# Performance work log

Hardware: AMD Instinct MI355X
Metric: run time of the kernel (lower is better)

Reference implementation:

```python
import jax, jax.numpy as jnp
import numpy as np

N = 8192        # batch_size == num nodes == num hyperedges
D = 512         # hidden_dim
H_HEADS = 8
HD = D // H_HEADS
TOP_K = 16
EPS = 1e-5      # LayerNorm eps


def setup_inputs() -> dict:
    key = jax.random.key(0)
    ks = jax.random.split(key, 10)
    def rn(k, shape, scale=0.02):
        return jax.random.normal(k, shape, dtype=jnp.float32) * scale
    return {
        "x0": jax.random.normal(ks[0], (N, D), dtype=jnp.float32),
        "x1": jax.random.normal(ks[1], (N, D), dtype=jnp.float32),
        # modality projections: Linear -> ReLU -> LayerNorm (per modality)
        "w_p0": rn(ks[2], (D, D)), "b_p0": jnp.zeros((D,), jnp.float32),
        "g0": jnp.ones((D,), jnp.float32), "beta0": jnp.zeros((D,), jnp.float32),
        "w_p1": rn(ks[3], (D, D)), "b_p1": jnp.zeros((D,), jnp.float32),
        "g1": jnp.ones((D,), jnp.float32), "beta1": jnp.zeros((D,), jnp.float32),
        # MultiheadAttention packed in-proj + out-proj
        "in_w": rn(ks[4], (3 * D, D)), "in_b": jnp.zeros((3 * D,), jnp.float32),
        "out_w": rn(ks[5], (D, D)), "out_b": jnp.zeros((D,), jnp.float32),
        # edge weight predictor MLP
        "ew_w1": rn(ks[6], (D // 2, D)), "ew_b1": jnp.zeros((D // 2,), jnp.float32),
        "ew_w2": rn(ks[7], (1, D // 2)), "ew_b2": jnp.zeros((1,), jnp.float32),
    }


def _layernorm(x, g, b):
    m = x.mean(-1, keepdims=True)
    v = ((x - m) ** 2).mean(-1, keepdims=True)
    return (x - m) * jax.lax.rsqrt(v + EPS) * g + b


def _forward(x0, x1, w_p0, b_p0, g0, beta0, w_p1, b_p1, g1, beta1,
             in_w, in_b, out_w, out_b, ew_w1, ew_b1, ew_w2, ew_b2):
    # per-modality projection: Linear -> ReLU -> LayerNorm
    p0 = _layernorm(jax.nn.relu(x0 @ w_p0.T + b_p0), g0, beta0)
    p1 = _layernorm(jax.nn.relu(x1 @ w_p1.T + b_p1), g1, beta1)
    seq = jnp.stack([p0, p1], axis=1)                       # [N, 2, D]
    # cross-modal MHA (self-attention over the 2 modality tokens)
    qkv = seq @ in_w.T + in_b                               # [N, 2, 3D]
    q, k, v = jnp.split(qkv, 3, axis=-1)
    q = q.reshape(N, 2, H_HEADS, HD)
    k = k.reshape(N, 2, H_HEADS, HD)
    v = v.reshape(N, 2, H_HEADS, HD)
    scores = jnp.einsum('bqhd,bkhd->bhqk', q, k) / jnp.sqrt(jnp.float32(HD))
    attn = jax.nn.softmax(scores, axis=-1)                  # [N, h, 2, 2]
    ctx = jnp.einsum('bhqk,bkhd->bqhd', attn, v).reshape(N, 2, D)
    attended = ctx @ out_w.T + out_b                        # [N, 2, D]
    fused = attended.mean(axis=1)                           # [N, D]
    # node-node attention similarity, row-softmax
    sim = jax.nn.softmax(fused @ fused.T, axis=1)           # [N, N]
    _, idx = jax.lax.top_k(sim, TOP_K)                      # [N, K]
    vals = jnp.take_along_axis(sim, idx, axis=1)            # [N, K]
    rows = jnp.arange(N)
    # H[i,i]=1 first, then H[neighbor, i] = sim[i, neighbor] (may overwrite diag)
    H = jnp.zeros((N, N), sim.dtype).at[rows, rows].set(1.0)
    H = H.at[idx, rows[:, None]].set(vals)
    colsum = H.sum(axis=0)
    H = H.at[rows, rows].set(jnp.where(colsum == 0, 1.0, H[rows, rows]))
    # edge weights
    hidden = jax.nn.relu(fused @ ew_w1.T + ew_b1)
    ew = jax.nn.sigmoid(hidden @ ew_w2.T + ew_b2)[:, 0]     # [N]
    ew = jnp.maximum(ew, 1e-8)
    return H, ew


def reference(x0, x1, w_p0, b_p0, g0, beta0, w_p1, b_p1, g1, beta1,
              in_w, in_b, out_w, out_b, ew_w1, ew_b1, ew_w2, ew_b2):
    return _forward(x0, x1, w_p0, b_p0, g0, beta0, w_p1, b_p1, g1, beta1,
                    in_w, in_b, out_w, out_b, ew_w1, ew_b1, ew_w2, ew_b2)
```

## Files before the change

### kernel.cpp

```cpp
#include <hip/hip_runtime.h>
#include <hip/hip_bf16.h>

#define NN 8192
#define DD 512

typedef unsigned short u16;
typedef __bf16 bf16_t;
typedef bf16_t bf16x8 __attribute__((ext_vector_type(8)));
typedef float f32x4 __attribute__((ext_vector_type(4)));

__device__ __forceinline__ float bf2f(u16 h) {
    union { unsigned u; float f; } v; v.u = ((unsigned)h) << 16; return v.f;
}
__device__ __forceinline__ float bflo(unsigned u) {
    union { unsigned u; float f; } v; v.u = u << 16; return v.f;
}
__device__ __forceinline__ float bfhi(unsigned u) {
    union { unsigned u; float f; } v; v.u = u & 0xFFFF0000u; return v.f;
}
__device__ __forceinline__ u16 f2bf(float f) {
    union { float f; unsigned u; } v; v.f = f;
    unsigned r = v.u + 0x7fffu + ((v.u >> 16) & 1u);
    return (u16)(r >> 16);
}

#define PIPE_BARRIER(N) do { \
    __builtin_amdgcn_sched_barrier(0); \
    asm volatile("s_waitcnt vmcnt(" #N ")" ::: "memory"); \
    __builtin_amdgcn_s_barrier(); \
    __builtin_amdgcn_sched_barrier(0); \
} while (0)

__global__ __launch_bounds__(256) void cvt5(
        const float* __restrict__ s0, u16* __restrict__ d0,
        const float* __restrict__ s1, u16* __restrict__ d1,
        const float* __restrict__ s2, u16* __restrict__ d2,
        const float* __restrict__ s3, u16* __restrict__ d3,
        const float* __restrict__ s4, u16* __restrict__ d4) {
    size_t v = ((size_t)blockIdx.x * 256 + threadIdx.x) * 8;
    const float* s; u16* d; size_t off;
    if (v < 262144)       { s = s0; d = d0; off = v; }
    else if (v < 524288)  { s = s1; d = d1; off = v - 262144; }
    else if (v < 1310720) { s = s2; d = d2; off = v - 524288; }
    else if (v < 1572864) { s = s3; d = d3; off = v - 1310720; }
    else                  { s = s4; d = d4; off = v - 1572864; }
    float4 a = *(const float4*)(s + off);
    float4 b = *(const float4*)(s + off + 4);
    ushort4 o0 = make_ushort4(f2bf(a.x), f2bf(a.y), f2bf(a.z), f2bf(a.w));
    ushort4 o1 = make_ushort4(f2bf(b.x), f2bf(b.y), f2bf(b.z), f2bf(b.w));
    *(ushort4*)(d + off) = o0;
    *(ushort4*)(d + off + 4) = o1;
}

#define EPS_LDS 136
__global__ __launch_bounds__(256) void gemm_proj(
        const float* __restrict__ X0, const float* __restrict__ X1,
        const u16* __restrict__ B0, const float* __restrict__ bias0,
        const u16* __restrict__ B1, const float* __restrict__ bias1,
        u16* __restrict__ C) {
    __shared__ alignas(16) u16 Smem[2][16384];
    const int t = threadIdx.x;
    const int lane = t & 63;
    const int wave = t >> 6;
    const int wm = (wave >> 1) * 64;
    const int wn = (wave & 1) * 64;
    const int rowA = blockIdx.y * 128;
    const int rowB = blockIdx.x * 128;
    const bool mod1 = (int)blockIdx.y >= 64;
    const float* A32 = mod1 ? X1 + (size_t)(rowA - 8192) * DD
                            : X0 + (size_t)rowA * DD;
    const u16* B = mod1 ? B1 : B0;
    const float* bias = mod1 ? bias1 : bias0;

    f32x4 acc[4][4] = {};
    const int mrow = lane & 15;
    const int kk = (lane >> 4) * 8;
    const int trow = t >> 3;
    const int koff = (t & 7) * 8;

    float ar[4][8];
    auto LOADA = [&](int k0) {
        #pragma unroll
        for (int r = 0; r < 4; ++r) {
            const float* s = A32 + (size_t)(r * 32 + trow) * DD + k0 + koff;
            float4 f0 = *(const float4*)s;
            float4 f1 = *(const float4*)(s + 4);
            ar[r][0] = f0.x; ar[r][1] = f0.y; ar[r][2] = f0.z; ar[r][3] = f0.w;
            ar[r][4] = f1.x; ar[r][5] = f1.y; ar[r][6] = f1.z; ar[r][7] = f1.w;
        }
    };
    auto WRITEA = [&](int buf) {
        u16* As = Smem[buf];
        #pragma unroll
        for (int r = 0; r < 4; ++r) {
            int chunk = r * 256 + t;
            ushort4 o0 = make_ushort4(f2bf(ar[r][0]), f2bf(ar[r][1]),
                                      f2bf(ar[r][2]), f2bf(ar[r][3]));
            ushort4 o1 = make_ushort4(f2bf(ar[r][4]), f2bf(ar[r][5]),
                                      f2bf(ar[r][6]), f2bf(ar[r][7]));
            *(ushort4*)(As + chunk * 8) = o0;
            *(ushort4*)(As + chunk * 8 + 4) = o1;
        }
    };
    auto BSTAGE = [&](int buf, int k0) {
        u16* Bs = Smem[buf] + 8192;
        #pragma unroll
        for (int r = 0; r < 4; ++r) {
            int chunk = r * 256 + t;
            const u16* srcB = B + (size_t)(rowB + (chunk >> 3)) * DD + k0 + (chunk & 7) * 8;
            __builtin_amdgcn_global_load_lds(
                (const __attribute__((address_space(1))) void*)srcB,
                (__attribute__((address_space(3))) void*)(Bs + chunk * 8), 16, 0, 0);
        }
    };

    LOADA(0); BSTAGE(0, 0); WRITEA(0);
    __syncthreads();
    int cur = 0;
    for (int ti = 0; ti < 8; ++ti) {
        if (ti < 7) { LOADA((ti + 1) << 6); BSTAGE(cur ^ 1, (ti + 1) << 6); }
        const u16* As = Smem[cur];
        const u16* Bs = Smem[cur] + 8192;
        #pragma unroll
        for (int ks = 0; ks < 64; ks += 32) {
            bf16x8 af[4], bfv[4];
            #pragma unroll
            for (int i = 0; i < 4; ++i)
                af[i] = *(const bf16x8*)(As + (wm + i * 16 + mrow) * 64 + ks + kk);
            #pragma unroll
            for (int j = 0; j < 4; ++j)
                bfv[j] = *(const bf16x8*)(Bs + (wn + j * 16 + mrow) * 64 + ks + kk);
            #pragma unroll
            for (int i = 0; i < 4; ++i)
                #pragma unroll
                for (int j = 0; j < 4; ++j)
                    acc[i][j] = __builtin_amdgcn_mfma_f32_16x16x32_bf16(af[i], bfv[j], acc[i][j], 0, 0, 0);
        }
        if (ti < 7) WRITEA(cur ^ 1);
        __syncthreads();
        cur ^= 1;
    }

    u16* Ep = &Smem[0][0];
    const int er0 = wm + (lane >> 4) * 4;
    const int ec0 = wn + (lane & 15);
    #pragma unroll
    for (int j = 0; j < 4; ++j) {
        int c = ec0 + j * 16;
        float bv = bias[rowB + c];
        #pragma unroll
        for (int i = 0; i < 4; ++i) {
            #pragma unroll
            for (int r = 0; r < 4; ++r) {
                float v = fmaxf(acc[i][j][r] + bv, 0.0f);
                Ep[(er0 + i * 16 + r) * EPS_LDS + c] = f2bf(v);
            }
        }
    }
    __syncthreads();
    #pragma unroll
    for (int pass = 0; pass < 8; ++pass) {
        int chunk = pass * 256 + t;
        int rloc = chunk >> 4, coff = (chunk & 15) * 8;
        bf16x8 v = *(const bf16x8*)(Ep + rloc * EPS_LDS + coff);
        *(bf16x8*)(C + (size_t)(rowA + rloc) * DD + rowB + coff) = v;
    }
}

__global__ __launch_bounds__(256) void gemm_qkv(const u16* __restrict__ A,
        const u16* __restrict__ B, const float* __restrict__ bias,
        u16* __restrict__ V, float* __restrict__ AL) {
    __shared__ alignas(16) u16 Smem[3][8192];
    const int t = threadIdx.x;
    const int lane = t & 63;
    const int wave = t >> 6;
    const int wm = (wave >> 1) * 64;
    const int wn = (wave & 1) * 64;
    const int c = blockIdx.x;
    const int rowA = blockIdx.y * 128;
    const bool isQK = (c < 8);

    f32x4 acc[4][4] = {};
    const int mrow = lane & 15;
    const int kk = (lane >> 4) * 8;

    auto STAGE = [&](int buf, int k0) {
        u16* As = Smem[buf];
        u16* Bs = Smem[buf] + 4096;
        #pragma unroll
        for (int r = 0; r < 2; ++r) {
            int chunk = r * 256 + t;
            int rr = chunk >> 2;
            int ko = (chunk & 3) * 8;
            int brow = isQK ? (c * 64 + rr + ((rr >= 64) ? 448 : 0))
                            : (1024 + (c - 8) * 128 + rr);
            const u16* srcA = A + (size_t)(rowA + rr) * DD + k0 + ko;
            __builtin_amdgcn_global_load_lds(
                (const __attribute__((address_space(1))) void*)srcA,
                (__attribute__((address_space(3))) void*)(As + chunk * 8), 16, 0, 0);
            const u16* srcB = B + (size_t)brow * DD + k0 + ko;
            __builtin_amdgcn_global_load_lds(
                (const __attribute__((address_space(1))) void*)srcB,
                (__attribute__((address_space(3))) void*)(Bs + chunk * 8), 16, 0, 0);
        }
    };
    auto COMPUTE = [&](int buf) {
        const u16* As = Smem[buf];
        const u16* Bs = Smem[buf] + 4096;
        bf16x8 af[4], bfv[4];
        #pragma unroll
        for (int i = 0; i < 4; ++i)
            af[i] = *(const bf16x8*)(As + (wm + i * 16 + mrow) * 32 + kk);
        #pragma unroll
        for (int j = 0; j < 4; ++j)
            bfv[j] = *(const bf16x8*)(Bs + (wn + j * 16 + mrow) * 32 + kk);
        #pragma unroll
        for (int i = 0; i < 4; ++i)
            #pragma unroll
            for (int j = 0; j < 4; ++j)
                acc[i][j] = __builtin_amdgcn_mfma_f32_16x16x32_bf16(af[i], bfv[j], acc[i][j], 0, 0, 0);
    };

    STAGE(0, 0);
    STAGE(1, 32);
    PIPE_BARRIER(4);
    #pragma unroll
    for (int ts = 0; ts < 14; ++ts) {
        STAGE((ts + 2) % 3, (ts + 2) * 32);
        COMPUTE(ts % 3);
        PIPE_BARRIER(4);
    }
    COMPUTE(2);
    PIPE_BARRIER(0);
    COMPUTE(0);
    __syncthreads();

    u16* Ep = &Smem[0][0];
    const int er0 = wm + (lane >> 4) * 4;
    const int ec0 = wn + (lane & 15);
    #pragma unroll
    for (int j = 0; j < 4; ++j) {
        int cc = ec0 + j * 16;
        int bcol = isQK ? ((cc < 64) ? c * 64 + cc : 448 + c * 64 + cc)
                        : (1024 + (c - 8) * 128 + cc);
        float bv = bias[bcol];
        #pragma unroll
        for (int i = 0; i < 4; ++i) {
            #pragma unroll
            for (int r = 0; r < 4; ++r)
                Ep[(er0 + i * 16 + r) * EPS_LDS + cc] = f2bf(acc[i][j][r] + bv);
        }
    }
    __syncthreads();
    if (isQK) {
        int nd = t >> 2, cb = t & 3, tt2 = cb >> 1, ss = cb & 1;
        const u16* qrow = Ep + (2 * nd + tt2) * EPS_LDS;
        const u16* krow = Ep + (2 * nd + ss) * EPS_LDS + 64;
        float s = 0.0f;
        #pragma unroll
        for (int d8 = 0; d8 < 8; ++d8) {
            bf16x8 qv = *(const bf16x8*)(qrow + d8 * 8);
            bf16x8 kv = *(const bf16x8*)(krow + d8 * 8);
            #pragma unroll
            for (int u = 0; u < 8; ++u) s += (float)qv[u] * (float)kv[u];
        }
        s *= 0.125f;
        float o = __shfl_xor(s, 1);
        float mm = fmaxf(s, o);
        float es = __expf(s - mm), eo = __expf(o - mm);
        float a = es / (es + eo);
        float a2 = __shfl_xor(a, 2);
        float al = 0.5f * (a + a2);
        if (cb < 2)
            AL[(size_t)(rowA / 2 + nd) * 16 + c * 2 + cb] = al;
    } else {
        #pragma unroll
        for (int pass = 0; pass < 8; ++pass) {
            int chunk = pass * 256 + t;
            int rloc = chunk >> 4, coff = (chunk & 15) * 8;
            bf16x8 v = *(const bf16x8*)(Ep + rloc * EPS_LDS + coff);
            *(bf16x8*)(V + (size_t)(rowA + rloc) * 512 + (c - 8) * 128 + coff) = v;
        }
    }
}

__global__ __launch_bounds__(256) void gemm_outp(
        const float* __restrict__ AL, const u16* __restrict__ V,
        const u16* __restrict__ W, const float* __restrict__ bias,
        u16* __restrict__ C) {
    __shared__ alignas(16) u16 Smem[2][16384];
    const int t = threadIdx.x;
    const int lane = t & 63;
    const int wave = t >> 6;
    const int wm = (wave >> 1) * 64;
    const int wn = (wave & 1) * 64;
    const int rowA = blockIdx.y * 128;
    const int rowB = blockIdx.x * 128;

    f32x4 acc[4][4] = {};
    const int mrow = lane & 15;
    const int kk = (lane >> 4) * 8;
    const int trow = t >> 3;
    const int koff = (t & 7) * 8;

    uint4 v0r[4], v1r[4];
    float2 alr[4];
    auto LOADA = [&](int ti) {
        #pragma unroll
        for (int r = 0; r < 4; ++r) {
            int node = rowA + r * 32 + trow;
            alr[r] = *(const float2*)(AL + (size_t)node * 16 + ti * 2);
            const u16* v0p = V + (size_t)(2 * node) * 512 + ti * 64 + koff;
            v0r[r] = *(const uint4*)v0p;
            v1r[r] = *(const uint4*)(v0p + 512);
        }
    };
    auto WRITEA = [&](int buf) {
        u16* As = Smem[buf];
        #pragma unroll
        for (int r = 0; r < 4; ++r) {
            int chunk = r * 256 + t;
            union { u16 us[8]; ushort4 u4[2]; } o;
            #pragma unroll
            for (int q = 0; q < 4; ++q) {
                unsigned w0 = (&v0r[r].x)[q], w1 = (&v1r[r].x)[q];
                o.us[q * 2]     = f2bf(alr[r].x * bflo(w0) + alr[r].y * bflo(w1));
                o.us[q * 2 + 1] = f2bf(alr[r].x * bfhi(w0) + alr[r].y * bfhi(w1));
            }
            *(ushort4*)(As + chunk * 8) = o.u4[0];
            *(ushort4*)(As + chunk * 8 + 4) = o.u4[1];
        }
    };
    auto BSTAGE = [&](int buf, int k0) {
        u16* Bs = Smem[buf] + 8192;
        #pragma unroll
        for (int r = 0; r < 4; ++r) {
            int chunk = r * 256 + t;
            const u16* srcB = W + (size_t)(rowB + (chunk >> 3)) * DD + k0 + (chunk & 7) * 8;
            __builtin_amdgcn_global_load_lds(
                (const __attribute__((address_space(1))) void*)srcB,
                (__attribute__((address_space(3))) void*)(Bs + chunk * 8), 16, 0, 0);
        }
    };

    LOADA(0); BSTAGE(0, 0); WRITEA(0);
    __syncthreads();
    int cur = 0;
    for (int ti = 0; ti < 8; ++ti) {
        if (ti < 7) { LOADA(ti + 1); BSTAGE(cur ^ 1, (ti + 1) << 6); }
        const u16* As = Smem[cur];
        const u16* Bs = Smem[cur] + 8192;
        #pragma unroll
        for (int ks = 0; ks < 64; ks += 32) {
            bf16x8 af[4], bfv[4];
            #pragma unroll
            for (int i = 0; i < 4; ++i)
                af[i] = *(const bf16x8*)(As + (wm + i * 16 + mrow) * 64 + ks + kk);
            #pragma unroll
            for (int j = 0; j < 4; ++j)
                bfv[j] = *(const bf16x8*)(Bs + (wn + j * 16 + mrow) * 64 + ks + kk);
            #pragma unroll
            for (int i = 0; i < 4; ++i)
                #pragma unroll
                for (int j = 0; j < 4; ++j)
                    acc[i][j] = __builtin_amdgcn_mfma_f32_16x16x32_bf16(af[i], bfv[j], acc[i][j], 0, 0, 0);
        }
        if (ti < 7) WRITEA(cur ^ 1);
        __syncthreads();
        cur ^= 1;
    }

    u16* Ep = &Smem[0][0];
    const int er0 = wm + (lane >> 4) * 4;
    const int ec0 = wn + (lane & 15);
    #pragma unroll
    for (int j = 0; j < 4; ++j) {
        int c = ec0 + j * 16;
        float bv = bias[rowB + c];
        #pragma unroll
        for (int i = 0; i < 4; ++i) {
            #pragma unroll
            for (int r = 0; r < 4; ++r)
                Ep[(er0 + i * 16 + r) * EPS_LDS + c] = f2bf(acc[i][j][r] + bv);
        }
    }
    __syncthreads();
    #pragma unroll
    for (int pass = 0; pass < 8; ++pass) {
        int chunk = pass * 256 + t;
        int rloc = chunk >> 4, coff = (chunk & 15) * 8;
        bf16x8 v = *(const bf16x8*)(Ep + rloc * EPS_LDS + coff);
        *(bf16x8*)(C + (size_t)(rowA + rloc) * DD + rowB + coff) = v;
    }
}

#define SYM_LDS 129
__global__ __launch_bounds__(256) void gemm_symh(const u16* __restrict__ F,
        u16* __restrict__ C, const u16* __restrict__ W1,
        const float* __restrict__ b1, u16* __restrict__ Hid) {
    __shared__ alignas(16) u16 Smem[3][8192];
    const int bx = blockIdx.x, by = blockIdx.y;
    const bool isHid = (bx >= 64);
    if (!isHid && bx < by) return;
    const int t = threadIdx.x;
    const int lane = t & 63;
    const int wave = t >> 6;
    const int wm = (wave >> 1) * 64;
    const int wn = (wave & 1) * 64;
    const int rowI = by * 128;
    const int rowJ = isHid ? (bx - 64) * 128 : bx * 128;
    const u16* Bsrc = isHid ? W1 : F;

    f32x4 acc[4][4] = {};
    const int mrow = lane & 15;
    const int kk = (lane >> 4) * 8;

    auto STAGE = [&](int buf, int k0) {
        u16* As = Smem[buf];
        u16* Bs = Smem[buf] + 4096;
        #pragma unroll
        for (int r = 0; r < 2; ++r) {
            int chunk = r * 256 + t;
            int row = chunk >> 2;
            int ko = (chunk & 3) * 8;
            const u16* srcA = F + (size_t)(rowI + row) * DD + k0 + ko;
            __builtin_amdgcn_global_load_lds(
                (const __attribute__((address_space(1))) void*)srcA,
                (__attribute__((address_space(3))) void*)(As + chunk * 8), 16, 0, 0);
            const u16* srcB = Bsrc + (size_t)(rowJ + row) * DD + k0 + ko;
            __builtin_amdgcn_global_load_lds(
                (const __attribute__((address_space(1))) void*)srcB,
                (__attribute__((address_space(3))) void*)(Bs + chunk * 8), 16, 0, 0);
        }
    };
    auto COMPUTE = [&](int buf) {
        const u16* As = Smem[buf];
        const u16* Bs = Smem[buf] + 4096;
        bf16x8 af[4], bfv[4];
        #pragma unroll
        for (int i = 0; i < 4; ++i)
            af[i] = *(const bf16x8*)(As + (wm + i * 16 + mrow) * 32 + kk);
        #pragma unroll
        for (int j = 0; j < 4; ++j)
            bfv[j] = *(const bf16x8*)(Bs + (wn + j * 16 + mrow) * 32 + kk);
        #pragma unroll
        for (int i = 0; i < 4; ++i)
            #pragma unroll
            for (int j = 0; j < 4; ++j)
                acc[i][j] = __builtin_amdgcn_mfma_f32_16x16x32_bf16(af[i], bfv[j], acc[i][j], 0, 0, 0);
    };

    STAGE(0, 0);
    STAGE(1, 32);
    PIPE_BARRIER(4);
    #pragma unroll
    for (int ts = 0; ts < 14; ++ts) {
        STAGE((ts + 2) % 3, (ts + 2) * 32);
        COMPUTE(ts % 3);
        PIPE_BARRIER(4);
    }
    COMPUTE(2);
    PIPE_BARRIER(0);
    COMPUTE(0);
    __syncthreads();

    u16* Ep = &Smem[0][0];
    const int er0 = wm + (lane >> 4) * 4;
    const int ec0 = wn + (lane & 15);
    #pragma unroll
    for (int j = 0; j < 4; ++j) {
        int c = ec0 + j * 16;
        float bv = isHid ? b1[rowJ + c] : 0.0f;
        #pragma unroll
        for (int i = 0; i < 4; ++i) {
            #pragma unroll
            for (int r = 0; r < 4; ++r) {
                float v = acc[i][j][r] + bv;
                if (isHid) v = fmaxf(v, 0.0f);
                Ep[(er0 + i * 16 + r) * SYM_LDS + c] = f2bf(v);
            }
        }
    }
    __syncthreads();
    if (isHid) {
        #pragma unroll
        for (int pass = 0; pass < 8; ++pass) {
            int chunk = pass * 256 + t;
            int rloc = chunk >> 4, coff = (chunk & 15) * 8;
            union { u16 us[8]; bf16x8 v; } buf;
            #pragma unroll
            for (int k = 0; k < 8; ++k) buf.us[k] = Ep[rloc * SYM_LDS + coff + k];
            *(bf16x8*)(Hid + (size_t)(rowI + rloc) * 256 + rowJ + coff) = buf.v;
        }
        return;
    }
    #pragma unroll
    for (int pass = 0; pass < 8; ++pass) {
        int chunk = pass * 256 + t;
        int rloc = chunk >> 4, coff = (chunk & 15) * 8;
        union { u16 us[8]; bf16x8 v; } buf;
        #pragma unroll
        for (int k = 0; k < 8; ++k) buf.us[k] = Ep[rloc * SYM_LDS + coff + k];
        *(bf16x8*)(C + (size_t)(rowI + rloc) * NN + rowJ + coff) = buf.v;
    }
    if (bx != by) {
        #pragma unroll
        for (int pass = 0; pass < 8; ++pass) {
            int chunk = pass * 256 + t;
            int tr = chunk >> 4, roff = (chunk & 15) * 8;
            union { u16 us[8]; bf16x8 v; } buf;
            #pragma unroll
            for (int k = 0; k < 8; ++k) buf.us[k] = Ep[(roff + k) * SYM_LDS + tr];
            *(bf16x8*)(C + (size_t)(rowJ + tr) * NN + rowI + roff) = buf.v;
        }
    }
}

__global__ __launch_bounds__(256) void ln2_kernel(const u16* __restrict__ y,
        const float* __restrict__ g0, const float* __restrict__ b0,
        const float* __restrict__ g1, const float* __restrict__ b1,
        u16* __restrict__ seq) {
    int n = blockIdx.x * 4 + (threadIdx.x >> 6);
    int lane = threadIdx.x & 63;
    int modality = n >> 13, node = n & (NN - 1);
    const float* g = modality ? g1 : g0;
    const float* b = modality ? b1 : b0;
    bf16x8 v = *(const bf16x8*)(y + (size_t)n * DD + lane * 8);
    float x[8];
    float s = 0.0f;
    #pragma unroll
    for (int u = 0; u < 8; ++u) { x[u] = (float)v[u]; s += x[u]; }
    #pragma unroll
    for (int off = 32; off; off >>= 1) s += __shfl_xor(s, off);
    float mean = s * (1.0f / DD);
    float vs = 0.0f;
    #pragma unroll
    for (int u = 0; u < 8; ++u) { x[u] -= mean; vs += x[u] * x[u]; }
    #pragma unroll
    for (int off = 32; off; off >>= 1) vs += __shfl_xor(vs, off);
    float inv = rsqrtf(vs * (1.0f / DD) + 1e-5f);
    float4 ga = *(const float4*)(g + lane * 8);
    float4 gb = *(const float4*)(g + lane * 8 + 4);
    float4 ba = *(const float4*)(b + lane * 8);
    float4 bb = *(const float4*)(b + lane * 8 + 4);
    union { u16 us[8]; bf16x8 v; } o;
    o.us[0] = f2bf(x[0] * inv * ga.x + ba.x);
    o.us[1] = f2bf(x[1] * inv * ga.y + ba.y);
    o.us[2] = f2bf(x[2] * inv * ga.z + ba.z);
    o.us[3] = f2bf(x[3] * inv * ga.w + ba.w);
    o.us[4] = f2bf(x[4] * inv * gb.x + bb.x);
    o.us[5] = f2bf(x[5] * inv * gb.y + bb.y);
    o.us[6] = f2bf(x[6] * inv * gb.z + bb.z);
    o.us[7] = f2bf(x[7] * inv * gb.w + bb.w);
    *(bf16x8*)(seq + (size_t)node * (2 * DD) + modality * DD + lane * 8) = o.v;
}

__global__ __launch_bounds__(256) void topk_bf16(u16* __restrict__ S,
        float* __restrict__ topv, int* __restrict__ topi,
        u16* __restrict__ hidden, const float* __restrict__ w2,
        const float* __restrict__ b2, float* __restrict__ ew_out,
        float* __restrict__ H) {
    const int blk = blockIdx.x;
    const int t = threadIdx.x;
    const float4 z4 = make_float4(0.f, 0.f, 0.f, 0.f);
    if (blk >= 2048) {
        int wv = t >> 6, lane = t & 63;
        int n0 = (blk - 2048) * 64 + wv * 16;
        float wa = w2[lane], wb = w2[lane + 64], wc = w2[lane + 128], wd = w2[lane + 192];
        for (int q = 0; q < 16; ++q) {
            int n = n0 + q;
            const u16* hr = hidden + (size_t)n * 256;
            float s = bf2f(hr[lane]) * wa + bf2f(hr[lane + 64]) * wb
                    + bf2f(hr[lane + 128]) * wc + bf2f(hr[lane + 192]) * wd;
            #pragma unroll
            for (int off = 32; off; off >>= 1) s += __shfl_xor(s, off);
            if (lane == 0) {
                float z = s + b2[0];
                float sig = 1.0f / (1.0f + __expf(-z));
                ew_out[n] = fmaxf(sig, 1e-8f);
            }
        }
        float4* zb = (float4*)(hidden + (size_t)n0 * 256);
        #pragma unroll
        for (int i = 0; i < 8; ++i) zb[i * 64 + lane] = z4;
        return;
    }
    const float NEG = -3e38f;
    const int SENT = 0x7FFFFFFF;
    int row = blk * 4 + (t >> 6);
    int lane = t & 63;
    u16* Sr = S + (size_t)row * NN;

    float m = NEG, l = 0.0f;
    float t1v = NEG, t2v = NEG, t3v = NEG;
    int t1i = SENT, t2i = SENT, t3i = SENT;

    #pragma unroll
    for (int p = 0; p < 16; ++p) {
        uint4 raw = *(const uint4*)(Sr + p * 512 + lane * 8);
        int base = p * 512 + lane * 8;
        #pragma unroll
        for (int q = 0; q < 4; ++q) {
            unsigned w = (&raw.x)[q];
            #pragma unroll
            for (int h = 0; h < 2; ++h) {
                float x = h ? bfhi(w) : bflo(w);
                int xi = base + q * 2 + h;
                if (x > m) { l = l * __expf(m - x) + 1.0f; m = x; }
                else l += __expf(x - m);
                bool g1 = x > t1v, g2 = x > t2v, g3 = x > t3v;
                t3v = g2 ? t2v : (g3 ? x : t3v);
                t3i = g2 ? t2i : (g3 ? xi : t3i);
                t2v = g1 ? t1v : (g2 ? x : t2v);
                t2i = g1 ? t1i : (g2 ? xi : t2i);
                t1v = g1 ? x : t1v;
                t1i = g1 ? xi : t1i;
            }
        }
    }
    #pragma unroll
    for (int off = 32; off; off >>= 1) {
        float om = __shfl_xor(m, off);
        float ol = __shfl_xor(l, off);
        float nm = fmaxf(m, om);
        l = l * __expf(m - nm) + ol * __expf(om - nm);
        m = nm;
    }

    unsigned mk0 = 0, mk1 = 0, mk2 = 0, mk3 = 0;
    float c1v = t1v, c2v = t2v, c3v = t3v;
    int c1i = t1i, c2i = t2i, c3i = t3i;
    for (int r = 0; r < 16; ++r) {
        float wv = c1v; int wi = c1i;
        #pragma unroll
        for (int off = 32; off; off >>= 1) {
            float ov = __shfl_xor(wv, off);
            int oi = __shfl_xor(wi, off);
            if (ov > wv || (ov == wv && oi < wi)) { wv = ov; wi = oi; }
        }
        if (lane == 0) {
            topv[(size_t)row * 16 + r] = __expf(wv - m) / l;
            topi[(size_t)row * 16 + r] = wi;
        }
        if (wi == c1i) {
            int slot = ((wi >> 9) << 3) | (wi & 7);
            unsigned bit = 1u << (slot & 31);
            if (slot < 32) mk0 |= bit; else if (slot < 64) mk1 |= bit;
            else if (slot < 96) mk2 |= bit; else mk3 |= bit;
            c1v = c2v; c1i = c2i;
            c2v = c3v; c2i = c3i;
            c3v = NEG; c3i = SENT;
            if (c1i == SENT) {
                float nb = NEG; int ni = SENT;
                #pragma unroll
                for (int p = 0; p < 16; ++p) {
                    uint4 raw = *(const uint4*)(Sr + p * 512 + lane * 8);
                    int base = p * 512 + lane * 8;
                    #pragma unroll
                    for (int q = 0; q < 4; ++q) {
                        unsigned w = (&raw.x)[q];
                        #pragma unroll
                        for (int h = 0; h < 2; ++h) {
                            int sl = p * 8 + q * 2 + h;
                            unsigned mw = (sl < 32) ? mk0 : (sl < 64) ? mk1
                                        : (sl < 96) ? mk2 : mk3;
                            float x = ((mw >> (sl & 31)) & 1u) ? NEG
                                    : (h ? bfhi(w) : bflo(w));
                            if (x > nb) { nb = x; ni = base + q * 2 + h; }
                        }
                    }
                }
                c1v = nb; c1i = ni;
            }
        }
    }

    float4* srow = (float4*)Sr;
    #pragma unroll
    for (int i = 0; i < 16; ++i) srow[i * 64 + lane] = z4;

    {
        size_t vb0 = (size_t)blk * 63488;
        #pragma unroll
        for (int rr = 0; rr < 16; ++rr) {
            int j = rr * 256 + t;
            if (j < 3968) {
                size_t b = vb0 + (size_t)j * 16;
                char* p = (char*)H + (b < 109051904u ? b : b + 4194304u);
                *(float4*)p = z4;
            }
        }
    }
}

__global__ __launch_bounds__(256) void scatter_diag(const float* __restrict__ topv,
        const int* __restrict__ topi, float* __restrict__ H) {
    int tk = blockIdx.x * 256 + threadIdx.x;
    if (tk < NN * 16) {
        int i = tk >> 4;
        int idx = topi[tk];
        H[(size_t)idx * NN + i] = topv[tk];
    } else {
        int c = tk - NN * 16;
        const int* ti = topi + c * 16;
        bool self = false;
        #pragma unroll
        for (int j = 0; j < 16; ++j) self |= (ti[j] == c);
        if (!self) H[(size_t)c * NN + c] = 1.0f;
    }
}

extern "C" void kernel_launch(void* const* d_in, const int* in_sizes, int n_in,
                              void* d_out, int out_size, void* d_ws, size_t ws_size,
                              hipStream_t stream) {
    const float* x0    = (const float*)d_in[0];
    const float* x1    = (const float*)d_in[1];
    const float* w_p0  = (const float*)d_in[2];
    const float* b_p0  = (const float*)d_in[3];
    const float* g0    = (const float*)d_in[4];
    const float* beta0 = (const float*)d_in[5];
    const float* w_p1  = (const float*)d_in[6];
    const float* b_p1  = (const float*)d_in[7];
    const float* g1    = (const float*)d_in[8];
    const float* beta1 = (const float*)d_in[9];
    const float* in_w  = (const float*)d_in[10];
    const float* in_b  = (const float*)d_in[11];
    const float* out_w = (const float*)d_in[12];
    const float* out_b = (const float*)d_in[13];
    const float* ew_w1 = (const float*)d_in[14];
    const float* ew_b1 = (const float*)d_in[15];
    const float* ew_w2 = (const float*)d_in[16];
    const float* ew_b2 = (const float*)d_in[17];

    float* Hf = (float*)d_out;
    float* ew_out = Hf + (size_t)NN * NN;

    u16* Hu = (u16*)d_out;
    u16* y01    = Hu + 8388608;
    u16* seq    = Hu + 16777216;
    u16* Vbuf   = Hu + 25165824;
    u16* hidden = Hu + 54525952;
    float* ALb  = (float*)(Hu + 58720256);
    u16* wp0b   = Hu + 60817408;
    u16* wp1b   = wp0b + 262144;
    u16* inwb   = wp1b + 262144;
    u16* outwb  = inwb + 786432;
    u16* eww1b  = outwb + 262144;
    u16* Sb     = Hu + 67108864;
    char* ws = (char*)d_ws;
    u16* fusedB = (u16*)ws;
    float* topv = (float*)(ws + (8u << 20));
    int*   topi = (int*)(ws + (8u << 20) + 524288);

    dim3 blk(256);
    cvt5<<<dim3(832), blk, 0, stream>>>(w_p0, wp0b, w_p1, wp1b,
                                        in_w, inwb, out_w, outwb, ew_w1, eww1b);
    gemm_proj<<<dim3(4, 128), blk, 0, stream>>>(
        x0, x1, wp0b, b_p0, wp1b, b_p1, y01);
    ln2_kernel<<<dim3(2 * NN / 4), blk, 0, stream>>>(y01, g0, beta0, g1, beta1, seq);
    gemm_qkv<<<dim3(12, 128), blk, 0, stream>>>(seq, inwb, in_b, Vbuf, ALb);
    gemm_outp<<<dim3(4, 64), blk, 0, stream>>>(ALb, Vbuf, outwb, out_b, fusedB);
    gemm_symh<<<dim3(66, 64), blk, 0, stream>>>(fusedB, Sb, eww1b, ew_b1, hidden);
    topk_bf16<<<dim3(2176), blk, 0, stream>>>(Sb, topv, topi,
        hidden, ew_w2, ew_b2, ew_out, Hf);
    scatter_diag<<<dim3((NN * 16 + NN) / 256), blk, 0, stream>>>(topv, topi, Hf);
}
```

Baseline: 570.8 us.

## Compute softmax row max/sum statistics in the similarity GEMM epilogue

Per-tile row and column softmax statistics (max and sum of exps) are now computed in the symmetric similarity GEMM epilogue from LDS, for both the tile and its transpose, and written to a scratch buffer at the start of the output. The top-k kernel no longer runs an online softmax per element; it reads the 64 partial stats per row and merges them with shuffles. The top-k kernel also zeroes the scratch region, and the H-zeroing offsets are adjusted around it. This removes exp work from the hot top-k scan at the cost of extra LDS reads, exps and global writes in the GEMM epilogue.

```diff
diff --git a/kernel.cpp b/kernel.cpp
--- a/kernel.cpp
+++ b/kernel.cpp
@@ -397,7 +397,8 @@
 #define SYM_LDS 129
 __global__ __launch_bounds__(256) void gemm_symh(const u16* __restrict__ F,
         u16* __restrict__ C, const u16* __restrict__ W1,
-        const float* __restrict__ b1, u16* __restrict__ Hid) {
+        const float* __restrict__ b1, u16* __restrict__ Hid,
+        float2* __restrict__ STz) {
     __shared__ alignas(16) u16 Smem[3][8192];
     const int bx = blockIdx.x, by = blockIdx.y;
     const bool isHid = (bx >= 64);
@@ -494,6 +495,40 @@
         }
         return;
     }
+
+    {
+        int r2 = t >> 1, hf = t & 1;
+        const u16* rp = Ep + r2 * SYM_LDS + hf * 64;
+        float mloc = -3e38f;
+        #pragma unroll 8
+        for (int i2 = 0; i2 < 64; ++i2) mloc = fmaxf(mloc, bf2f(rp[i2]));
+        float mt = fmaxf(mloc, __shfl_xor(mloc, 1));
+        float l0 = 0.0f, l1 = 0.0f;
+        #pragma unroll 8
+        for (int i2 = 0; i2 < 64; i2 += 2) {
+            l0 += __expf(bf2f(rp[i2]) - mt);
+            l1 += __expf(bf2f(rp[i2 + 1]) - mt);
+        }
+        float lt = l0 + l1 + __shfl_xor(l0 + l1, 1);
+        if (hf == 0) STz[(size_t)(rowI + r2) * 64 + bx] = make_float2(mt, lt);
+    }
+    if (bx != by) {
+        int c2 = t >> 1, hf = t & 1;
+        const u16* cp = Ep + (hf * 64) * SYM_LDS + c2;
+        float mloc = -3e38f;
+        #pragma unroll 8
+        for (int i2 = 0; i2 < 64; ++i2) mloc = fmaxf(mloc, bf2f(cp[i2 * SYM_LDS]));
+        float mt = fmaxf(mloc, __shfl_xor(mloc, 1));
+        float l0 = 0.0f, l1 = 0.0f;
+        #pragma unroll 8
+        for (int i2 = 0; i2 < 64; i2 += 2) {
+            l0 += __expf(bf2f(cp[i2 * SYM_LDS]) - mt);
+            l1 += __expf(bf2f(cp[(i2 + 1) * SYM_LDS]) - mt);
+        }
+        float lt = l0 + l1 + __shfl_xor(l0 + l1, 1);
+        if (hf == 0) STz[(size_t)(rowJ + c2) * 64 + by] = make_float2(mt, lt);
+    }
+
     #pragma unroll
     for (int pass = 0; pass < 8; ++pass) {
         int chunk = pass * 256 + t;
@@ -557,9 +592,9 @@
 
 __global__ __launch_bounds__(256) void topk_bf16(u16* __restrict__ S,
         float* __restrict__ topv, int* __restrict__ topi,
-        u16* __restrict__ hidden, const float* __restrict__ w2,
-        const float* __restrict__ b2, float* __restrict__ ew_out,
-        float* __restrict__ H) {
+        float2* __restrict__ STz, u16* __restrict__ hidden,
+        const float* __restrict__ w2, const float* __restrict__ b2,
+        float* __restrict__ ew_out, float* __restrict__ H) {
     const int blk = blockIdx.x;
     const int t = threadIdx.x;
     const float4 z4 = make_float4(0.f, 0.f, 0.f, 0.f);
@@ -591,7 +626,6 @@
     int lane = t & 63;
     u16* Sr = S + (size_t)row * NN;
 
-    float m = NEG, l = 0.0f;
     float t1v = NEG, t2v = NEG, t3v = NEG;
     int t1i = SENT, t2i = SENT, t3i = SENT;
 
@@ -606,8 +640,6 @@
             for (int h = 0; h < 2; ++h) {
                 float x = h ? bfhi(w) : bflo(w);
                 int xi = base + q * 2 + h;
-                if (x > m) { l = l * __expf(m - x) + 1.0f; m = x; }
-                else l += __expf(x - m);
                 bool g1 = x > t1v, g2 = x > t2v, g3 = x > t3v;
                 t3v = g2 ? t2v : (g3 ? x : t3v);
                 t3i = g2 ? t2i : (g3 ? xi : t3i);
@@ -618,6 +650,8 @@
             }
         }
     }
+    float2 st = STz[(size_t)row * 64 + lane];
+    float m = st.x, l = st.y;
     #pragma unroll
     for (int off = 32; off; off >>= 1) {
         float om = __shfl_xor(m, off);
@@ -678,17 +712,15 @@
     float4* srow = (float4*)Sr;
     #pragma unroll
     for (int i = 0; i < 16; ++i) srow[i * 64 + lane] = z4;
+    STz[(size_t)row * 64 + lane] = make_float2(0.f, 0.f);
 
     {
-        size_t vb0 = (size_t)blk * 63488;
-        #pragma unroll
-        for (int rr = 0; rr < 16; ++rr) {
-            int j = rr * 256 + t;
-            if (j < 3968) {
-                size_t b = vb0 + (size_t)j * 16;
-                char* p = (char*)H + (b < 109051904u ? b : b + 4194304u);
-                *(float4*)p = z4;
-            }
+        size_t vb0 = 4194304u + (size_t)blk * 61440;
+        #pragma unroll
+        for (int rr = 0; rr < 15; ++rr) {
+            size_t b = vb0 + (size_t)(rr * 256 + t) * 16;
+            char* p = (char*)H + (b < 109051904u ? b : b + 4194304u);
+            *(float4*)p = z4;
         }
     }
 }
@@ -736,6 +768,7 @@
     float* ew_out = Hf + (size_t)NN * NN;
 
     u16* Hu = (u16*)d_out;
+    float2* STz = (float2*)Hu;
     u16* y01    = Hu + 8388608;
     u16* seq    = Hu + 16777216;
     u16* Vbuf   = Hu + 25165824;
@@ -760,8 +793,9 @@
     ln2_kernel<<<dim3(2 * NN / 4), blk, 0, stream>>>(y01, g0, beta0, g1, beta1, seq);
     gemm_qkv<<<dim3(12, 128), blk, 0, stream>>>(seq, inwb, in_b, Vbuf, ALb);
     gemm_outp<<<dim3(4, 64), blk, 0, stream>>>(ALb, Vbuf, outwb, out_b, fusedB);
-    gemm_symh<<<dim3(66, 64), blk, 0, stream>>>(fusedB, Sb, eww1b, ew_b1, hidden);
-    topk_bf16<<<dim3(2176), blk, 0, stream>>>(Sb, topv, topi,
+    gemm_symh<<<dim3(66, 64), blk, 0, stream>>>(fusedB, Sb, eww1b, ew_b1,
+                                                hidden, STz);
+    topk_bf16<<<dim3(2176), blk, 0, stream>>>(Sb, topv, topi, STz,
         hidden, ew_w2, ew_b2, ew_out, Hf);
     scatter_diag<<<dim3((NN * 16 + NN) / 256), blk, 0, stream>>>(topv, topi, Hf);
 }
```

Result: slower. 589.4 us (+3.3%).
